# Performance work log

Measured on AMD Instinct MI355X. Metric: run time of the kernel, lower is better.

The kernel has to match this reference:

```python
import jax, jax.numpy as jnp
import numpy as np

N_NODES = 10000
N_EDGES = 160000
NEG_SLOPE = 0.2
DIMS = [(128, 1024), (1024, 512), (512, 128)]
NUM_CLASSES = 64


def _glorot(k, shape):
    lim = np.sqrt(6.0 / (shape[0] + shape[1])).astype(np.float32)
    return jax.random.uniform(k, shape, jnp.float32, -lim, lim)


def setup_inputs() -> dict:
    key = jax.random.key(0)
    ks = iter(jax.random.split(key, 32))
    inp = {
        'x': jax.random.normal(next(ks), (N_NODES, DIMS[0][0]), jnp.float32),
        'edge_index': jax.random.randint(next(ks), (2, N_EDGES), 0, N_NODES, jnp.int64),
    }
    for i, (fin, fout) in enumerate(DIMS, start=1):
        inp[f'Wl{i}'] = _glorot(next(ks), (fin, fout))
        inp[f'bl{i}'] = jnp.zeros((fout,), jnp.float32)
        inp[f'Wr{i}'] = _glorot(next(ks), (fin, fout))
        inp[f'br{i}'] = jnp.zeros((fout,), jnp.float32)
        inp[f'att{i}'] = _glorot(next(ks), (1, fout))[0]
        inp[f'b{i}'] = jnp.zeros((fout,), jnp.float32)
    inp['Wc'] = _glorot(next(ks), (DIMS[-1][1], NUM_CLASSES))
    inp['bc'] = jnp.zeros((NUM_CLASSES,), jnp.float32)
    return inp


def _gatv2(x, src, dst, Wl, bl, Wr, br, att, b):
    # PyG GATv2Conv, heads=1, add_self_loops=True (self-loops appended by caller)
    n = x.shape[0]
    xl = x @ Wl + bl          # source-side transform [N, F]
    xr = x @ Wr + br          # target-side transform [N, F]
    m = xl[src] + xr[dst]     # [E, F] per-edge message
    e = jax.nn.leaky_relu(m, NEG_SLOPE) @ att  # [E] attention logits
    # segment softmax over incoming edges of each dst node
    emax = jax.ops.segment_max(e, dst, num_segments=n)
    ez = jnp.exp(e - emax[dst])
    denom = jax.ops.segment_sum(ez, dst, num_segments=n)
    alpha = ez / denom[dst]
    out = jax.ops.segment_sum(alpha[:, None] * xl[src], dst, num_segments=n)
    return out + b


def reference(x, edge_index, Wl1, bl1, Wr1, br1, att1, b1,
              Wl2, bl2, Wr2, br2, att2, b2,
              Wl3, bl3, Wr3, br3, att3, b3, Wc, bc):
    n = x.shape[0]
    loops = jnp.arange(n, dtype=edge_index.dtype)
    src = jnp.concatenate([edge_index[0], loops])
    dst = jnp.concatenate([edge_index[1], loops])
    h = jax.nn.relu(_gatv2(x, src, dst, Wl1, bl1, Wr1, br1, att1, b1))
    h = jax.nn.relu(_gatv2(h, src, dst, Wl2, bl2, Wr2, br2, att2, b2))
    h = jax.nn.relu(_gatv2(h, src, dst, Wl3, bl3, Wr3, br3, att3, b3))
    return h @ Wc + bc
```

## Files before the change

### kernel.cpp

```cpp
#include <hip/hip_runtime.h>


typedef __attribute__((ext_vector_type(8))) short bf16x8;
typedef __attribute__((ext_vector_type(4))) float f32x4;

__device__ __forceinline__ unsigned short bf16rn(float x) {
    union { float f; unsigned int u; } v; v.f = x;
    unsigned int r = v.u + 0x7FFF + ((v.u >> 16) & 1);
    return (unsigned short)(r >> 16);
}
__device__ __forceinline__ float bf16tof(unsigned short h) {
    union { unsigned int u; float f; } v; v.u = ((unsigned int)h) << 16;
    return v.f;
}

typedef __attribute__((address_space(1))) const void* gptr_t;
typedef __attribute__((address_space(3))) void* sptr_t;
__device__ __forceinline__ void gload_lds16(const void* g, void* l) {
    __builtin_amdgcn_global_load_lds((gptr_t)g, (sptr_t)l, 16, 0, 0);
}


__global__ __launch_bounds__(256) void splitT_kernel(
    const float* __restrict__ W, unsigned short* __restrict__ Th,
    unsigned short* __restrict__ Tl, int K, int F)
{
    __shared__ float tile[32][33];
    const int tx = threadIdx.x & 31, ty = threadIdx.x >> 5;
    const int k0 = blockIdx.x * 32, f0 = blockIdx.y * 32;
#pragma unroll
    for (int i = 0; i < 32; i += 8)
        tile[ty + i][tx] = W[(size_t)(k0 + ty + i) * F + f0 + tx];
    __syncthreads();
#pragma unroll
    for (int i = 0; i < 32; i += 8) {
        int f = f0 + ty + i, k = k0 + tx;
        float v = tile[tx][ty + i];
        unsigned short h = bf16rn(v);
        Th[(size_t)f * K + k] = h;
        Tl[(size_t)f * K + k] = bf16rn(v - bf16tof(h));
    }
}

__global__ void split_kernel(const float* __restrict__ X,
                             unsigned short* __restrict__ Hi,
                             unsigned short* __restrict__ Lo, int n4)
{
    int i = blockIdx.x * blockDim.x + threadIdx.x;
    if (i >= n4) return;
    float4 v = ((const float4*)X)[i];
    ushort4 h, l;
    h.x = bf16rn(v.x); l.x = bf16rn(v.x - bf16tof(h.x));
    h.y = bf16rn(v.y); l.y = bf16rn(v.y - bf16tof(h.y));
    h.z = bf16rn(v.z); l.z = bf16rn(v.z - bf16tof(h.z));
    h.w = bf16rn(v.w); l.w = bf16rn(v.w - bf16tof(h.w));
    ((ushort4*)Hi)[i] = h;
    ((ushort4*)Lo)[i] = l;
}


__global__ __launch_bounds__(256) void gemm2_mfma_kernel(
    const unsigned short* __restrict__ Ahi, const unsigned short* __restrict__ Alo,
    int M, int K,
    const unsigned short* __restrict__ WThA, const unsigned short* __restrict__ WTlA,
    const unsigned short* __restrict__ WThB, const unsigned short* __restrict__ WTlB,
    const float* __restrict__ biasA, const float* __restrict__ biasB,
    float* __restrict__ CA, float* __restrict__ CB, int F)
{
    __shared__ unsigned short Ash[128 * 32];
    __shared__ unsigned short Asl[128 * 32];
    __shared__ unsigned short Bsh[128 * 32];
    __shared__ unsigned short Bsl[128 * 32];

    const int t = threadIdx.x;
    const int lane = t & 63, wave = t >> 6;
    const int nyh = (int)gridDim.y >> 1;
    const int half = ((int)blockIdx.y >= nyh) ? 1 : 0;
    const int colBase = ((int)blockIdx.y - half * nyh) * 128;
    const unsigned short* WTh = half ? WThB : WThA;
    const unsigned short* WTl = half ? WTlB : WTlA;
    const float* bias = half ? biasB : biasA;
    float* C = half ? CB : CA;
    const int rowBase = (int)blockIdx.x * 128;

    const int wr = wave >> 1, wc = wave & 1;
    const int fr = lane & 15, g = lane >> 4;

    const int srow = lane >> 2;
    const int schunk = (lane & 3) * 8;
    const int r0 = wave * 16 + srow;
    const int r1 = (wave + 4) * 16 + srow;
    int ga0 = rowBase + r0; if (ga0 > M - 1) ga0 = M - 1;
    int ga1 = rowBase + r1; if (ga1 > M - 1) ga1 = M - 1;

    const unsigned short* pAh0 = Ahi + (size_t)ga0 * K + schunk;
    const unsigned short* pAh1 = Ahi + (size_t)ga1 * K + schunk;
    const unsigned short* pAl0 = Alo + (size_t)ga0 * K + schunk;
    const unsigned short* pAl1 = Alo + (size_t)ga1 * K + schunk;
    const unsigned short* pBh0 = WTh + (size_t)(colBase + r0) * K + schunk;
    const unsigned short* pBh1 = WTh + (size_t)(colBase + r1) * K + schunk;
    const unsigned short* pBl0 = WTl + (size_t)(colBase + r0) * K + schunk;
    const unsigned short* pBl1 = WTl + (size_t)(colBase + r1) * K + schunk;

    unsigned short* dAh0 = &Ash[wave * 512];
    unsigned short* dAh1 = &Ash[(wave + 4) * 512];
    unsigned short* dAl0 = &Asl[wave * 512];
    unsigned short* dAl1 = &Asl[(wave + 4) * 512];
    unsigned short* dBh0 = &Bsh[wave * 512];
    unsigned short* dBh1 = &Bsh[(wave + 4) * 512];
    unsigned short* dBl0 = &Bsl[wave * 512];
    unsigned short* dBl1 = &Bsl[(wave + 4) * 512];

    f32x4 acc[4][4];
#pragma unroll
    for (int i = 0; i < 4; ++i)
#pragma unroll
        for (int j = 0; j < 4; ++j) acc[i][j] = (f32x4)(0.f);

    for (int k0 = 0; k0 < K; k0 += 32) {
        gload_lds16(pAh0 + k0, dAh0);
        gload_lds16(pAh1 + k0, dAh1);
        gload_lds16(pAl0 + k0, dAl0);
        gload_lds16(pAl1 + k0, dAl1);
        gload_lds16(pBh0 + k0, dBh0);
        gload_lds16(pBh1 + k0, dBh1);
        gload_lds16(pBl0 + k0, dBl0);
        gload_lds16(pBl1 + k0, dBl1);
        __syncthreads();

        bf16x8 ah[4], al[4], bh[4], bl[4];
#pragma unroll
        for (int mi = 0; mi < 4; ++mi) {
            ah[mi] = *(const bf16x8*)&Ash[(wr * 64 + mi * 16 + fr) * 32 + g * 8];
            al[mi] = *(const bf16x8*)&Asl[(wr * 64 + mi * 16 + fr) * 32 + g * 8];
        }
#pragma unroll
        for (int ni = 0; ni < 4; ++ni) {
            bh[ni] = *(const bf16x8*)&Bsh[(wc * 64 + ni * 16 + fr) * 32 + g * 8];
            bl[ni] = *(const bf16x8*)&Bsl[(wc * 64 + ni * 16 + fr) * 32 + g * 8];
        }
#pragma unroll
        for (int mi = 0; mi < 4; ++mi)
#pragma unroll
            for (int ni = 0; ni < 4; ++ni) {
                acc[mi][ni] = __builtin_amdgcn_mfma_f32_16x16x32_bf16(ah[mi], bh[ni], acc[mi][ni], 0, 0, 0);
                acc[mi][ni] = __builtin_amdgcn_mfma_f32_16x16x32_bf16(ah[mi], bl[ni], acc[mi][ni], 0, 0, 0);
                acc[mi][ni] = __builtin_amdgcn_mfma_f32_16x16x32_bf16(al[mi], bh[ni], acc[mi][ni], 0, 0, 0);
            }
        __syncthreads();
    }

#pragma unroll
    for (int mi = 0; mi < 4; ++mi) {
        const int row0 = rowBase + wr * 64 + mi * 16 + g * 4;
#pragma unroll
        for (int ni = 0; ni < 4; ++ni) {
            const int col = colBase + wc * 64 + ni * 16 + fr;
            const float b = bias[col];
#pragma unroll
            for (int r = 0; r < 4; ++r) {
                const int row = row0 + r;
                if (row < M) C[(size_t)row * F + col] = acc[mi][ni][r] + b;
            }
        }
    }
}


static constexpr int BM = 64, BN = 64, BK = 16;

__global__ __launch_bounds__(256) void gemm_bias_kernel(
    const float* __restrict__ A, const float* __restrict__ W,
    const float* __restrict__ bias, float* __restrict__ C,
    int M, int K, int F)
{
    __shared__ float As[BK][BM];
    __shared__ float Bs[BK][BN];
    const int t = threadIdx.x;
    const int bm = blockIdx.x, bn = blockIdx.y;
    const int ty = t >> 4, tx = t & 15;
    const int rowBase = bm * BM;
    const int colBase = bn * BN;
    const int aRow = t & 63;
    const int aK = (t >> 6) << 2;
    const int gARow = min(rowBase + aRow, M - 1);
    const int bRow = t >> 4;
    const int bCol = (t & 15) << 2;

    float acc[4][4] = {{0.f, 0.f, 0.f, 0.f}};

    for (int k0 = 0; k0 < K; k0 += BK) {
        float4 av = *(const float4*)&A[(size_t)gARow * K + k0 + aK];
        float4 bv = *(const float4*)&W[(size_t)(k0 + bRow) * F + colBase + bCol];
        As[aK + 0][aRow] = av.x;
        As[aK + 1][aRow] = av.y;
        As[aK + 2][aRow] = av.z;
        As[aK + 3][aRow] = av.w;
        *(float4*)&Bs[bRow][bCol] = bv;
        __syncthreads();
#pragma unroll
        for (int kk = 0; kk < BK; ++kk) {
            float4 a4 = *(const float4*)&As[kk][ty << 2];
            float4 b4 = *(const float4*)&Bs[kk][tx << 2];
            float ar[4] = {a4.x, a4.y, a4.z, a4.w};
            float br_[4] = {b4.x, b4.y, b4.z, b4.w};
#pragma unroll
            for (int i = 0; i < 4; ++i)
#pragma unroll
                for (int j = 0; j < 4; ++j)
                    acc[i][j] += ar[i] * br_[j];
        }
        __syncthreads();
    }

    float4 bias4 = *(const float4*)&bias[colBase + (tx << 2)];
    float bb[4] = {bias4.x, bias4.y, bias4.z, bias4.w};
#pragma unroll
    for (int i = 0; i < 4; ++i) {
        int r = rowBase + (ty << 2) + i;
        if (r < M) {
            float4 o;
            o.x = acc[i][0] + bb[0];
            o.y = acc[i][1] + bb[1];
            o.z = acc[i][2] + bb[2];
            o.w = acc[i][3] + bb[3];
            *(float4*)&C[(size_t)r * F + colBase + (tx << 2)] = o;
        }
    }
}


__global__ void zero_ints_kernel(int* __restrict__ p, int n)
{
    int i = blockIdx.x * blockDim.x + threadIdx.x;
    if (i < n) p[i] = 0;
}

__device__ inline void edge_src_dst(const int* __restrict__ ei, int edge,
                                    int E_orig, int& src, int& dst)
{
    if (edge < E_orig) {
        src = ei[edge];
        dst = ei[E_orig + edge];
    } else {
        src = dst = edge - E_orig;
    }
}

__global__ void count_kernel(const int* __restrict__ ei, int E_orig, int E_tot,
                             int* __restrict__ counts)
{
    int e = blockIdx.x * blockDim.x + threadIdx.x;
    if (e >= E_tot) return;
    int src, dst;
    edge_src_dst(ei, e, E_orig, src, dst);
    atomicAdd(&counts[dst], 1);
}

__global__ __launch_bounds__(256) void scan_kernel(const int* __restrict__ counts, int n,
                                                   int* __restrict__ offsets,
                                                   int* __restrict__ cursor)
{
    __shared__ int part[256];
    const int t = threadIdx.x;
    const int chunk = (n + 255) >> 8;
    const int begin = t * chunk;
    const int end = min(begin + chunk, n);
    int s = 0;
    for (int i = begin; i < end; ++i) s += counts[i];
    part[t] = s;
    __syncthreads();
    for (int off = 1; off < 256; off <<= 1) {
        int v = (t >= off) ? part[t - off] : 0;
        __syncthreads();
        part[t] += v;
        __syncthreads();
    }
    int run = (t == 0) ? 0 : part[t - 1];
    for (int i = begin; i < end; ++i) {
        offsets[i] = run;
        cursor[i] = run;
        run += counts[i];
    }
    if (t == 255) offsets[n] = part[255];
}

__global__ void fill_kernel(const int* __restrict__ ei, int E_orig, int E_tot,
                            int* __restrict__ cursor, int* __restrict__ csr_src)
{
    int e = blockIdx.x * blockDim.x + threadIdx.x;
    if (e >= E_tot) return;
    int src, dst;
    edge_src_dst(ei, e, E_orig, src, dst);
    int pos = atomicAdd(&cursor[dst], 1);
    csr_src[pos] = src;
}


template<int F, int NTHREADS>
__global__ __launch_bounds__(NTHREADS) void fused_gat_kernel(
    const float* __restrict__ xl, const float* __restrict__ xr,
    const float* __restrict__ att, const int* __restrict__ offsets,
    const int* __restrict__ csr_src, const float* __restrict__ bias,
    float* __restrict__ out_f32,
    unsigned short* __restrict__ out_hi, unsigned short* __restrict__ out_lo)
{
    constexpr int VEC = F / NTHREADS;
    constexpr int NW = NTHREADS / 64;
    const int n = blockIdx.x;
    const int t = threadIdx.x;
    const int start = offsets[n], end = offsets[n + 1];

    __shared__ float wsum[2][NW > 1 ? NW : 1];

    float xr_r[VEC], att_r[VEC], acc[VEC];
#pragma unroll
    for (int v = 0; v < VEC; ++v) {
        xr_r[v]  = xr[(size_t)n * F + t * VEC + v];
        att_r[v] = att[t * VEC + v];
        acc[v]   = 0.f;
    }

    float m = -1e30f, d = 0.f;
    int parity = 0;

    for (int i = start; i < end; ++i, parity ^= 1) {
        const int src = csr_src[i];
        const float* row = xl + (size_t)src * F + t * VEC;
        float xlv[VEC];
        if constexpr (VEC == 4) {
            float4 v4 = *(const float4*)row;
            xlv[0] = v4.x; xlv[1] = v4.y; xlv[2] = v4.z; xlv[3] = v4.w;
        } else {
            float2 v2 = *(const float2*)row;
            xlv[0] = v2.x; xlv[1] = v2.y;
        }
        float p = 0.f;
#pragma unroll
        for (int v = 0; v < VEC; ++v) {
            float mm = xlv[v] + xr_r[v];
            mm = (mm >= 0.f) ? mm : 0.2f * mm;
            p += mm * att_r[v];
        }
#pragma unroll
        for (int off = 32; off; off >>= 1) p += __shfl_xor(p, off);
        float e;
        if constexpr (NW > 1) {
            if ((t & 63) == 0) wsum[parity][t >> 6] = p;
            __syncthreads();
            e = wsum[parity][0];
#pragma unroll
            for (int w = 1; w < NW; ++w) e += wsum[parity][w];
        } else {
            e = p;
        }
        const float nm = fmaxf(m, e);
        const float scale = __expf(m - nm);
        const float wgt = __expf(e - nm);
        d = d * scale + wgt;
#pragma unroll
        for (int v = 0; v < VEC; ++v) acc[v] = acc[v] * scale + wgt * xlv[v];
        m = nm;
    }

    const float inv = 1.0f / d;
#pragma unroll
    for (int v = 0; v < VEC; ++v) {
        const size_t idx = (size_t)n * F + t * VEC + v;
        float o = fmaxf(acc[v] * inv + bias[t * VEC + v], 0.f);
        if (out_f32) out_f32[idx] = o;
        if (out_hi) {
            unsigned short h = bf16rn(o);
            out_hi[idx] = h;
            out_lo[idx] = bf16rn(o - bf16tof(h));
        }
    }
}


extern "C" void kernel_launch(void* const* d_in, const int* in_sizes, int n_in,
                              void* d_out, int out_size, void* d_ws, size_t ws_size,
                              hipStream_t stream)
{
    const float* x   = (const float*)d_in[0];
    const int*   ei  = (const int*)d_in[1];
    const float* Wl1 = (const float*)d_in[2];
    const float* bl1 = (const float*)d_in[3];
    const float* Wr1 = (const float*)d_in[4];
    const float* br1 = (const float*)d_in[5];
    const float* at1 = (const float*)d_in[6];
    const float* b1  = (const float*)d_in[7];
    const float* Wl2 = (const float*)d_in[8];
    const float* bl2 = (const float*)d_in[9];
    const float* Wr2 = (const float*)d_in[10];
    const float* br2 = (const float*)d_in[11];
    const float* at2 = (const float*)d_in[12];
    const float* b2  = (const float*)d_in[13];
    const float* Wl3 = (const float*)d_in[14];
    const float* bl3 = (const float*)d_in[15];
    const float* Wr3 = (const float*)d_in[16];
    const float* br3 = (const float*)d_in[17];
    const float* at3 = (const float*)d_in[18];
    const float* b3  = (const float*)d_in[19];
    const float* Wc  = (const float*)d_in[20];
    const float* bc  = (const float*)d_in[21];

    const int N = in_sizes[0] / 128;
    const int E_orig = in_sizes[1] / 2;
    const int E_tot = E_orig + N;

    size_t off = 0;
    auto alloc = [&](size_t bytes) -> char* {
        char* p = (char*)d_ws + off;
        off += (bytes + 255) & ~(size_t)255;
        return p;
    };
    float* bufA = (float*)alloc((size_t)N * 1024 * 4);
    float* bufB = (float*)alloc((size_t)N * 1024 * 4);
    unsigned short* S_hi = (unsigned short*)alloc((size_t)N * 1024 * 2);
    unsigned short* S_lo = (unsigned short*)alloc((size_t)N * 1024 * 2);
    unsigned short* WThl = (unsigned short*)alloc((size_t)524288 * 2);
    unsigned short* WTll = (unsigned short*)alloc((size_t)524288 * 2);
    unsigned short* WThr = (unsigned short*)alloc((size_t)524288 * 2);
    unsigned short* WTlr = (unsigned short*)alloc((size_t)524288 * 2);
    int* counts  = (int*)alloc((size_t)N * 4);
    int* offsets = (int*)alloc((size_t)(N + 1) * 4);
    int* cursor  = (int*)alloc((size_t)N * 4);
    int* csr_src = (int*)alloc((size_t)E_tot * 4);
    (void)ws_size; (void)n_in; (void)out_size;

    const int eb = (E_tot + 255) / 256;
    const int mb128 = (N + 127) / 128;

    zero_ints_kernel<<<(N + 255) / 256, 256, 0, stream>>>(counts, N);
    count_kernel<<<eb, 256, 0, stream>>>(ei, E_orig, E_tot, counts);
    scan_kernel<<<1, 256, 0, stream>>>(counts, N, offsets, cursor);
    fill_kernel<<<eb, 256, 0, stream>>>(ei, E_orig, E_tot, cursor, csr_src);

    split_kernel<<<(N * 128 / 4 + 255) / 256, 256, 0, stream>>>(x, S_hi, S_lo, N * 128 / 4);

    splitT_kernel<<<dim3(128 / 32, 1024 / 32), 256, 0, stream>>>(Wl1, WThl, WTll, 128, 1024);
    splitT_kernel<<<dim3(128 / 32, 1024 / 32), 256, 0, stream>>>(Wr1, WThr, WTlr, 128, 1024);
    gemm2_mfma_kernel<<<dim3(mb128, 16), 256, 0, stream>>>(
        S_hi, S_lo, N, 128, WThl, WTll, WThr, WTlr, bl1, br1, bufA, bufB, 1024);
    fused_gat_kernel<1024, 256><<<N, 256, 0, stream>>>(
        bufA, bufB, at1, offsets, csr_src, b1, nullptr, S_hi, S_lo);

    splitT_kernel<<<dim3(1024 / 32, 512 / 32), 256, 0, stream>>>(Wl2, WThl, WTll, 1024, 512);
    splitT_kernel<<<dim3(1024 / 32, 512 / 32), 256, 0, stream>>>(Wr2, WThr, WTlr, 1024, 512);
    gemm2_mfma_kernel<<<dim3(mb128, 8), 256, 0, stream>>>(
        S_hi, S_lo, N, 1024, WThl, WTll, WThr, WTlr, bl2, br2, bufA, bufB, 512);
    fused_gat_kernel<512, 128><<<N, 128, 0, stream>>>(
        bufA, bufB, at2, offsets, csr_src, b2, nullptr, S_hi, S_lo);

    splitT_kernel<<<dim3(512 / 32, 128 / 32), 256, 0, stream>>>(Wl3, WThl, WTll, 512, 128);
    splitT_kernel<<<dim3(512 / 32, 128 / 32), 256, 0, stream>>>(Wr3, WThr, WTlr, 512, 128);
    gemm2_mfma_kernel<<<dim3(mb128, 2), 256, 0, stream>>>(
        S_hi, S_lo, N, 512, WThl, WTll, WThr, WTlr, bl3, br3, bufA, bufB, 128);
    fused_gat_kernel<128, 64><<<N, 64, 0, stream>>>(
        bufA, bufB, at3, offsets, csr_src, b3, bufB, nullptr, nullptr);

    gemm_bias_kernel<<<dim3((N + BM - 1) / BM, 64 / BN), 256, 0, stream>>>(
        bufB, Wc, bc, (float*)d_out, N, 128, 64);
}
```

Baseline: 449.2 us.

## Assign one wavefront per node in GAT aggregation with prefetched rows

Replaces the block-per-node GAT aggregation kernel with one where each 64-lane wavefront handles a whole node and a block covers four nodes. This removes the per-edge __syncthreads and shared-memory cross-wave reduction, and it prefetches the next neighbor row into registers while the current one is processed. Output stores are also vectorized. In exchange each lane holds many more values (16 per array for F=1024), which raises register pressure and may lower occupancy, and per-node parallelism drops to one wave.

```diff
diff --git a/kernel.cpp b/kernel.cpp
--- a/kernel.cpp
+++ b/kernel.cpp
@@ -297,82 +297,108 @@
 }
 
 
-template<int F, int NTHREADS>
-__global__ __launch_bounds__(NTHREADS) void fused_gat_kernel(
+template<int F, bool SPLIT>
+__global__ __launch_bounds__(256) void fused_gat_wave_kernel(
     const float* __restrict__ xl, const float* __restrict__ xr,
     const float* __restrict__ att, const int* __restrict__ offsets,
     const int* __restrict__ csr_src, const float* __restrict__ bias,
     float* __restrict__ out_f32,
-    unsigned short* __restrict__ out_hi, unsigned short* __restrict__ out_lo)
-{
-    constexpr int VEC = F / NTHREADS;
-    constexpr int NW = NTHREADS / 64;
-    const int n = blockIdx.x;
-    const int t = threadIdx.x;
+    unsigned short* __restrict__ out_hi, unsigned short* __restrict__ out_lo,
+    int N)
+{
+    constexpr int VEC = F / 64;
+    constexpr int CW = (VEC >= 4) ? 4 : VEC;
+    constexpr int NC = VEC / CW;
+    const int wave = threadIdx.x >> 6, lane = threadIdx.x & 63;
+    const int n = blockIdx.x * 4 + wave;
+    if (n >= N) return;
     const int start = offsets[n], end = offsets[n + 1];
 
-    __shared__ float wsum[2][NW > 1 ? NW : 1];
-
-    float xr_r[VEC], att_r[VEC], acc[VEC];
-#pragma unroll
-    for (int v = 0; v < VEC; ++v) {
-        xr_r[v]  = xr[(size_t)n * F + t * VEC + v];
-        att_r[v] = att[t * VEC + v];
-        acc[v]   = 0.f;
-    }
-
+    float xr_r[VEC], att_r[VEC], acc[VEC], cur[VEC], nxt[VEC];
+
+#pragma unroll
+    for (int j = 0; j < NC; ++j)
+#pragma unroll
+        for (int c = 0; c < CW; ++c) {
+            const int f = j * 64 * CW + lane * CW + c;
+            xr_r[j * CW + c] = xr[(size_t)n * F + f];
+            att_r[j * CW + c] = att[f];
+            acc[j * CW + c] = 0.f;
+        }
+
+    auto loadrow = [&](const float* __restrict__ row, float* dst) {
+#pragma unroll
+        for (int j = 0; j < NC; ++j) {
+            if constexpr (CW == 4) {
+                float4 v = *(const float4*)&row[j * 256 + lane * 4];
+                dst[j * 4 + 0] = v.x; dst[j * 4 + 1] = v.y;
+                dst[j * 4 + 2] = v.z; dst[j * 4 + 3] = v.w;
+            } else {
+                float2 v = *(const float2*)&row[lane * 2];
+                dst[0] = v.x; dst[1] = v.y;
+            }
+        }
+    };
+
+    loadrow(xl + (size_t)csr_src[start] * F, cur);
     float m = -1e30f, d = 0.f;
-    int parity = 0;
-
-    for (int i = start; i < end; ++i, parity ^= 1) {
-        const int src = csr_src[i];
-        const float* row = xl + (size_t)src * F + t * VEC;
-        float xlv[VEC];
-        if constexpr (VEC == 4) {
-            float4 v4 = *(const float4*)row;
-            xlv[0] = v4.x; xlv[1] = v4.y; xlv[2] = v4.z; xlv[3] = v4.w;
-        } else {
-            float2 v2 = *(const float2*)row;
-            xlv[0] = v2.x; xlv[1] = v2.y;
-        }
+
+    for (int i = start; i < end; ++i) {
+        if (i + 1 < end) loadrow(xl + (size_t)csr_src[i + 1] * F, nxt);
         float p = 0.f;
 #pragma unroll
         for (int v = 0; v < VEC; ++v) {
-            float mm = xlv[v] + xr_r[v];
+            float mm = cur[v] + xr_r[v];
             mm = (mm >= 0.f) ? mm : 0.2f * mm;
             p += mm * att_r[v];
         }
 #pragma unroll
         for (int off = 32; off; off >>= 1) p += __shfl_xor(p, off);
-        float e;
-        if constexpr (NW > 1) {
-            if ((t & 63) == 0) wsum[parity][t >> 6] = p;
-            __syncthreads();
-            e = wsum[parity][0];
-#pragma unroll
-            for (int w = 1; w < NW; ++w) e += wsum[parity][w];
+        const float nm = fmaxf(m, p);
+        const float scale = __expf(m - nm);
+        const float wgt = __expf(p - nm);
+        d = d * scale + wgt;
+#pragma unroll
+        for (int v = 0; v < VEC; ++v) acc[v] = acc[v] * scale + wgt * cur[v];
+        m = nm;
+#pragma unroll
+        for (int v = 0; v < VEC; ++v) cur[v] = nxt[v];
+    }
+
+    const float inv = 1.0f / d;
+#pragma unroll
+    for (int j = 0; j < NC; ++j) {
+        float o[CW];
+#pragma unroll
+        for (int c = 0; c < CW; ++c) {
+            const int f = j * 64 * CW + lane * CW + c;
+            o[c] = fmaxf(acc[j * CW + c] * inv + bias[f], 0.f);
+        }
+        const size_t base = (size_t)n * F + j * 64 * CW + lane * CW;
+        if constexpr (SPLIT) {
+            if constexpr (CW == 4) {
+                ushort4 h, l;
+                h.x = bf16rn(o[0]); l.x = bf16rn(o[0] - bf16tof(h.x));
+                h.y = bf16rn(o[1]); l.y = bf16rn(o[1] - bf16tof(h.y));
+                h.z = bf16rn(o[2]); l.z = bf16rn(o[2] - bf16tof(h.z));
+                h.w = bf16rn(o[3]); l.w = bf16rn(o[3] - bf16tof(h.w));
+                *(ushort4*)&out_hi[base] = h;
+                *(ushort4*)&out_lo[base] = l;
+            } else {
+                ushort2 h, l;
+                h.x = bf16rn(o[0]); l.x = bf16rn(o[0] - bf16tof(h.x));
+                h.y = bf16rn(o[1]); l.y = bf16rn(o[1] - bf16tof(h.y));
+                *(ushort2*)&out_hi[base] = h;
+                *(ushort2*)&out_lo[base] = l;
+            }
         } else {
-            e = p;
-        }
-        const float nm = fmaxf(m, e);
-        const float scale = __expf(m - nm);
-        const float wgt = __expf(e - nm);
-        d = d * scale + wgt;
-#pragma unroll
-        for (int v = 0; v < VEC; ++v) acc[v] = acc[v] * scale + wgt * xlv[v];
-        m = nm;
-    }
-
-    const float inv = 1.0f / d;
-#pragma unroll
-    for (int v = 0; v < VEC; ++v) {
-        const size_t idx = (size_t)n * F + t * VEC + v;
-        float o = fmaxf(acc[v] * inv + bias[t * VEC + v], 0.f);
-        if (out_f32) out_f32[idx] = o;
-        if (out_hi) {
-            unsigned short h = bf16rn(o);
-            out_hi[idx] = h;
-            out_lo[idx] = bf16rn(o - bf16tof(h));
+            if constexpr (CW == 4) {
+                float4 v = {o[0], o[1], o[2], o[3]};
+                *(float4*)&out_f32[base] = v;
+            } else {
+                float2 v = {o[0], o[1]};
+                *(float2*)&out_f32[base] = v;
+            }
         }
     }
 }
@@ -431,6 +457,7 @@
 
     const int eb = (E_tot + 255) / 256;
     const int mb128 = (N + 127) / 128;
+    const int nb4 = (N + 3) / 4;
 
     zero_ints_kernel<<<(N + 255) / 256, 256, 0, stream>>>(counts, N);
     count_kernel<<<eb, 256, 0, stream>>>(ei, E_orig, E_tot, counts);
@@ -443,22 +470,22 @@
     splitT_kernel<<<dim3(128 / 32, 1024 / 32), 256, 0, stream>>>(Wr1, WThr, WTlr, 128, 1024);
     gemm2_mfma_kernel<<<dim3(mb128, 16), 256, 0, stream>>>(
         S_hi, S_lo, N, 128, WThl, WTll, WThr, WTlr, bl1, br1, bufA, bufB, 1024);
-    fused_gat_kernel<1024, 256><<<N, 256, 0, stream>>>(
-        bufA, bufB, at1, offsets, csr_src, b1, nullptr, S_hi, S_lo);
+    fused_gat_wave_kernel<1024, true><<<nb4, 256, 0, stream>>>(
+        bufA, bufB, at1, offsets, csr_src, b1, nullptr, S_hi, S_lo, N);
 
     splitT_kernel<<<dim3(1024 / 32, 512 / 32), 256, 0, stream>>>(Wl2, WThl, WTll, 1024, 512);
     splitT_kernel<<<dim3(1024 / 32, 512 / 32), 256, 0, stream>>>(Wr2, WThr, WTlr, 1024, 512);
     gemm2_mfma_kernel<<<dim3(mb128, 8), 256, 0, stream>>>(
         S_hi, S_lo, N, 1024, WThl, WTll, WThr, WTlr, bl2, br2, bufA, bufB, 512);
-    fused_gat_kernel<512, 128><<<N, 128, 0, stream>>>(
-        bufA, bufB, at2, offsets, csr_src, b2, nullptr, S_hi, S_lo);
+    fused_gat_wave_kernel<512, true><<<nb4, 256, 0, stream>>>(
+        bufA, bufB, at2, offsets, csr_src, b2, nullptr, S_hi, S_lo, N);
 
     splitT_kernel<<<dim3(512 / 32, 128 / 32), 256, 0, stream>>>(Wl3, WThl, WTll, 512, 128);
     splitT_kernel<<<dim3(512 / 32, 128 / 32), 256, 0, stream>>>(Wr3, WThr, WTlr, 512, 128);
     gemm2_mfma_kernel<<<dim3(mb128, 2), 256, 0, stream>>>(
         S_hi, S_lo, N, 512, WThl, WTll, WThr, WTlr, bl3, br3, bufA, bufB, 128);
-    fused_gat_kernel<128, 64><<<N, 64, 0, stream>>>(
-        bufA, bufB, at3, offsets, csr_src, b3, bufB, nullptr, nullptr);
+    fused_gat_wave_kernel<128, false><<<nb4, 256, 0, stream>>>(
+        bufA, bufB, at3, offsets, csr_src, b3, bufB, nullptr, nullptr, N);
 
     gemm_bias_kernel<<<dim3((N + BM - 1) / BM, 64 / BN), 256, 0, stream>>>(
         bufB, Wc, bc, (float*)d_out, N, 128, 64);
```

Measured after the change: 461.5 us. +2.7%, slower.
